# Kernel optimization log

Hardware: AMD Instinct MI355X
Metric: run time of the kernel (lower is better)

The kernel has to match this reference:

```python
import jax, jax.numpy as jnp
import numpy as np

N = 50000          # nodes
E = 800000         # edges (avg in-degree 16)
NFEAT, F = 128, 64 # input feat, hidden width (outfeat = outd_1 = outd_2 = 64)
ALPHA = 0.2        # leaky relu slope
AVG_LIN = 16.0             # sum(bin*hist)/N for deg histogram (all deg 16)
AVG_LOG = float(np.log(17.0))  # sum(log(bin+1)*hist)/N


def setup_inputs():
    key = jax.random.key(0)
    ks = jax.random.split(key, 16)
    g = lambda i, shp, s: (jax.random.normal(ks[i], shp, jnp.float32) * s)
    return {
        "x": g(0, (N, NFEAT), 1.0),
        "adj": jnp.zeros((1,), jnp.float32),
        "edge_index": jax.random.randint(ks[1], (2, E), 0, N, dtype=jnp.int32),
        "W0": g(2, (NFEAT, F), NFEAT ** -0.5), "b0": jnp.zeros((F,), jnp.float32),
        "c1_pre_W": g(3, (2 * F, F), (2 * F) ** -0.5), "c1_pre_b": jnp.zeros((F,), jnp.float32),
        "c1_post_W": g(4, (5 * F, F), (5 * F) ** -0.5), "c1_post_b": jnp.zeros((F,), jnp.float32),
        "c1_lin_W": g(5, (F, F), F ** -0.5), "c1_lin_b": jnp.zeros((F,), jnp.float32),
        "c2_pre_W": g(6, (2 * F, F), (2 * F) ** -0.5), "c2_pre_b": jnp.zeros((F,), jnp.float32),
        "c2_post_W": g(7, (5 * F, F), (5 * F) ** -0.5), "c2_post_b": jnp.zeros((F,), jnp.float32),
        "c2_lin_W": g(8, (F, F), F ** -0.5), "c2_lin_b": jnp.zeros((F,), jnp.float32),
        "W2": g(9, (F, 1), F ** -0.5), "b2": jnp.zeros((1,), jnp.float32),
    }


def pna_conv(x, src, dst, pre_W, pre_b, post_W, post_b, lin_W, lin_b):
    # message: pre_nn(cat[x_i, x_j]) per edge  (x_i = target, x_j = source)
    h = jnp.concatenate([x[dst], x[src]], axis=-1) @ pre_W + pre_b  # [E, F]
    cnt = jax.ops.segment_sum(jnp.ones((h.shape[0],), h.dtype), dst, num_segments=N)
    deg = jnp.clip(cnt, 1.0)                                        # [N]
    mean = jax.ops.segment_sum(h, dst, num_segments=N) / deg[:, None]
    mx = jax.ops.segment_max(h, dst, num_segments=N)
    mx = jnp.where(cnt[:, None] > 0, mx, 0.0)                       # empty segs -> 0
    agg = jnp.concatenate([mean, mx], axis=-1)                      # [N, 2F]
    att = agg * (AVG_LOG / jnp.log(deg + 1.0))[:, None]             # attenuation scaler
    lin = agg * (deg / AVG_LIN)[:, None]                            # linear scaler
    out = jnp.concatenate([x, att, lin], axis=-1)                   # [N, 5F]
    out = out @ post_W + post_b
    return out @ lin_W + lin_b


def reference(x, adj, edge_index, W0, b0,
              c1_pre_W, c1_pre_b, c1_post_W, c1_post_b, c1_lin_W, c1_lin_b,
              c2_pre_W, c2_pre_b, c2_post_W, c2_post_b, c2_lin_W, c2_lin_b,
              W2, b2):
    src, dst = edge_index[0], edge_index[1]
    h = jax.nn.leaky_relu(x @ W0 + b0, negative_slope=ALPHA)  # dropout = id (eval)
    h = jax.nn.relu(pna_conv(h, src, dst, c1_pre_W, c1_pre_b, c1_post_W, c1_post_b, c1_lin_W, c1_lin_b))
    h = jax.nn.relu(pna_conv(h, src, dst, c2_pre_W, c2_pre_b, c2_post_W, c2_post_b, c2_lin_W, c2_lin_b))
    return h @ W2 + b2  # [N, 1]
```

## Files before the change

kernel.cpp:

```cpp
#include <hip/hip_runtime.h>
#include <hip/hip_bf16.h>

typedef __hip_bfloat16 bf16;
typedef unsigned short u16;
typedef unsigned int u32;
typedef __attribute__((ext_vector_type(8))) short short8;
typedef __attribute__((ext_vector_type(4))) float f32x4;

static constexpr float AVG_LOG_C = 2.8332133440562162f;
#define BCAP 4096
#define CHUNK 8192

__device__ __forceinline__ u32 f2bf_bits(float f) {
    u32 u = __float_as_uint(f);
    return (u + 0x7fffu + ((u >> 16) & 1u)) >> 16;
}
__device__ __forceinline__ float bf2f(u16 b) {
    return __uint_as_float(((u32)b) << 16);
}

__global__ __launch_bounds__(1024) void detect_zero_kernel(
    const u32* __restrict__ xwords, int* __restrict__ flag,
    int* __restrict__ bcnt, int nb) {
    if (blockIdx.x == 0) {
        int tid = threadIdx.x;
        if (tid < 64) {
            int good = 0;
            for (int i = tid; i < 2048; i += 64) {
                u32 lo = xwords[i] & 0xffffu;
                float v = __uint_as_float(lo << 16);
                float a = fabsf(v);
                if (v == 0.0f || (a >= 1e-3f && a <= 100.0f)) good++;
            }
            for (int off = 32; off; off >>= 1) good += __shfl_xor(good, off, 64);
            if (tid == 0) *flag = (2 * good > 2048) ? 1 : 0;
        }
    } else {
        int i = (blockIdx.x - 1) * 1024 + threadIdx.x;
        if (i < nb) bcnt[i] = 0;
    }
}

__global__ void prep_kernel(
    const void* __restrict__ W0r,  const void* __restrict__ b0r,
    const void* __restrict__ pre1r, const void* __restrict__ preb1r,
    const void* __restrict__ post1r, const void* __restrict__ postb1r,
    const void* __restrict__ lin1r, const void* __restrict__ linb1r,
    const void* __restrict__ pre2r, const void* __restrict__ preb2r,
    const void* __restrict__ post2r, const void* __restrict__ postb2r,
    const void* __restrict__ lin2r, const void* __restrict__ linb2r,
    const void* __restrict__ W2r,  const void* __restrict__ b2r,
    u16* __restrict__ W0p, u16* __restrict__ pre1p, u16* __restrict__ pre2p,
    u16* __restrict__ wf1p, u16* __restrict__ wf2p,
    float* __restrict__ bfo1, float* __restrict__ bfo2,
    float* __restrict__ preb1f, float* __restrict__ preb2f,
    float* __restrict__ b0f, float* __restrict__ W2f, float* __restrict__ b2f,
    const int* __restrict__ flag) {
    int idx = blockIdx.x * 256 + threadIdx.x;
    bool isbf = (*flag) != 0;
    auto ld = [&](const void* p, int i) -> float {
        return isbf ? bf2f(((const u16*)p)[i]) : ((const float*)p)[i];
    };
    if (idx < 8192) {
        int j = idx & 7, l = (idx >> 3) & 63, tt = idx >> 9;
        int c = tt & 3, s = tt >> 2;
        int kk = s * 32 + (l >> 4) * 8 + j;
        int col = c * 16 + (l & 15);
        W0p[idx] = (u16)f2bf_bits(ld(W0r, kk * 64 + col));
        return;
    }
    idx -= 8192;
    for (int which = 0; which < 2; ++which) {
        if (idx < 8192) {
            const void* src = which ? pre2r : pre1r;
            u16* dst = which ? pre2p : pre1p;
            int j = idx & 7, l = (idx >> 3) & 63, tt = idx >> 9;
            int c = tt & 7, s = tt >> 3;
            int kk = s * 32 + (l >> 4) * 8 + j;
            int col = c * 16 + (l & 15);
            float v = (col < 64) ? ld(src, kk * 64 + col)
                                 : ld(src, (64 + kk) * 64 + (col - 64));
            dst[idx] = (u16)f2bf_bits(v);
            return;
        }
        idx -= 8192;
    }
    for (int which = 0; which < 2; ++which) {
        if (idx < 20480) {
            const void* postW = which ? post2r : post1r;
            const void* linW  = which ? lin2r  : lin1r;
            u16* dst = which ? wf2p : wf1p;
            int j = idx & 7, l = (idx >> 3) & 63, tt = idx >> 9;
            int c = tt & 3, s = tt >> 2;
            int kk = s * 32 + (l >> 4) * 8 + j;
            int col = c * 16 + (l & 15);
            float a = 0.f;
            for (int k = 0; k < 64; ++k)
                a = fmaf(ld(postW, kk * 64 + k), ld(linW, k * 64 + col), a);
            dst[idx] = (u16)f2bf_bits(a);
            return;
        }
        idx -= 20480;
    }
    for (int which = 0; which < 2; ++which) {
        if (idx < 64) {
            const void* postb = which ? postb2r : postb1r;
            const void* linW  = which ? lin2r : lin1r;
            const void* linb  = which ? linb2r : linb1r;
            float* dst = which ? bfo2 : bfo1;
            float a = ld(linb, idx);
            for (int k = 0; k < 64; ++k)
                a = fmaf(ld(postb, k), ld(linW, k * 64 + idx), a);
            dst[idx] = a;
            return;
        }
        idx -= 64;
    }
    if (idx < 64) { preb1f[idx] = ld(preb1r, idx); return; }
    idx -= 64;
    if (idx < 64) { preb2f[idx] = ld(preb2r, idx); return; }
    idx -= 64;
    if (idx < 64) { b0f[idx] = ld(b0r, idx); return; }
    idx -= 64;
    if (idx < 64) { W2f[idx] = ld(W2r, idx); return; }
    idx -= 64;
    if (idx < 1) { b2f[0] = ld(b2r, 0); }
}
#define PREP_TOTAL (8192 * 3 + 20480 * 2 + 64 * 6 + 1)

__global__ __launch_bounds__(1024) void bucket_scatter_kernel(
    const int* __restrict__ srcs, const int* __restrict__ dsts,
    int* __restrict__ bcnt, u32* __restrict__ bstage, int e, int nb) {
    __shared__ int lhist[1024];
    __shared__ int lbase[1024];
    int tid = threadIdx.x;
    int cbase = blockIdx.x * CHUNK;
    for (int b = tid; b < nb; b += 1024) lhist[b] = 0;
    __syncthreads();
#pragma unroll
    for (int i = 0; i < CHUNK; i += 1024) {
        int e0 = cbase + i + tid;
        if (e0 < e) atomicAdd(&lhist[dsts[e0] >> 7], 1);
    }
    __syncthreads();
    for (int b = tid; b < nb; b += 1024) {
        int c = lhist[b];
        lbase[b] = c ? atomicAdd(&bcnt[b], c) : 0;
        lhist[b] = 0;
    }
    __syncthreads();
#pragma unroll
    for (int i = 0; i < CHUNK; i += 1024) {
        int e0 = cbase + i + tid;
        if (e0 < e) {
            int d = dsts[e0];
            int b = d >> 7;
            int pos = lbase[b] + atomicAdd(&lhist[b], 1);
            if (pos < BCAP)
                bstage[(size_t)b * BCAP + pos] = (u32)srcs[e0] | ((u32)(d & 127) << 17);
        }
    }
}

__global__ __launch_bounds__(256) void bucket_build_kernel(
    const u32* __restrict__ bstage, const int* __restrict__ bcnt,
    int* __restrict__ rowptr, int* __restrict__ elist, int nb, int n) {
    __shared__ int hist[128];
    __shared__ int hoff[128];
    __shared__ int sbase;
    int b = blockIdx.x, tid = threadIdx.x;
    int lane = tid & 63;
    if (tid == 0) sbase = 0;
    if (tid < 128) hist[tid] = 0;
    __syncthreads();
    int part = 0;
    for (int k = tid; k < b; k += 256) part += min(bcnt[k], BCAP);
    for (int off = 32; off; off >>= 1) part += __shfl_xor(part, off, 64);
    if (lane == 0 && part) atomicAdd(&sbase, part);
    int cb = min(bcnt[b], BCAP);
    const u32* st = bstage + (size_t)b * BCAP;
    for (int i = tid; i < cb; i += 256) atomicAdd(&hist[st[i] >> 17], 1);
    __syncthreads();
    int base = sbase;
    if (tid == 0) {
        int run = 0;
        for (int j = 0; j < 128; ++j) { hoff[j] = run; run += hist[j]; }
    }
    __syncthreads();
    if (tid < 128) {
        int node = b * 128 + tid;
        if (node < n) rowptr[node] = base + hoff[tid];
        hist[tid] = hoff[tid];
    }
    if (b == nb - 1 && tid == 255) rowptr[n] = base + cb;
    __syncthreads();
    for (int i = tid; i < cb; i += 256) {
        u32 e = st[i];
        int pos = atomicAdd(&hist[e >> 17], 1);
        elist[base + pos] = (int)(e & 0x1ffffu);
    }
}

__global__ __launch_bounds__(1024) void gemm_x_pq_kernel(
    const void* __restrict__ xraw, const u16* __restrict__ W0p,
    const float* __restrict__ b0f, const u16* __restrict__ pre1p,
    u16* __restrict__ hA, u16* __restrict__ PQ,
    const int* __restrict__ flag, int n) {
    __shared__ __align__(16) u16 xsh[64 * 136];
    __shared__ __align__(16) u16 hsh[64 * 72];
    int tid = threadIdx.x;
    int wave = __builtin_amdgcn_readfirstlane(tid >> 6);
    int lane = tid & 63;
    int blockbase = blockIdx.x * 64;
    bool isbf = (*flag) != 0;
    {
        int row = tid >> 4;
        int cg = (tid & 15) * 8;
        int grow = blockbase + row;
        short8 v = short8{0, 0, 0, 0, 0, 0, 0, 0};
        if (grow < n) {
            if (isbf) {
                v = *(const short8*)((const u16*)xraw + (size_t)grow * 128 + cg);
            } else {
                const float* xf = (const float*)xraw + (size_t)grow * 128 + cg;
                f32x4 a0 = *(const f32x4*)xf;
                f32x4 a1 = *(const f32x4*)(xf + 4);
#pragma unroll
                for (int j = 0; j < 4; ++j) {
                    v[j]     = (short)f2bf_bits(a0[j]);
                    v[4 + j] = (short)f2bf_bits(a1[j]);
                }
            }
        }
        *(short8*)&xsh[row * 136 + cg] = v;
    }
    __syncthreads();
    int rt = wave & 3, ct = wave >> 2;
    int arl = rt * 16 + (lane & 15);
    int koff = (lane >> 4) * 8;
    f32x4 acc = f32x4{0.f, 0.f, 0.f, 0.f};
#pragma unroll
    for (int s = 0; s < 4; ++s) {
        short8 a = *(const short8*)&xsh[arl * 136 + s * 32 + koff];
        short8 b = *(const short8*)(W0p + ((size_t)(s * 4 + ct) * 64 + lane) * 8);
        acc = __builtin_amdgcn_mfma_f32_16x16x32_bf16(a, b, acc, 0, 0, 0);
    }
    {
        int col = ct * 16 + (lane & 15);
        float bv = b0f[col];
        int r0l = rt * 16 + (lane >> 4) * 4;
#pragma unroll
        for (int r = 0; r < 4; ++r) {
            float v = acc[r] + bv;
            v = v > 0.f ? v : 0.2f * v;
            u16 bits = (u16)f2bf_bits(v);
            hsh[(r0l + r) * 72 + col] = bits;
            int grow = blockbase + r0l + r;
            if (grow < n) hA[(size_t)grow * 64 + col] = bits;
        }
    }
    __syncthreads();
#pragma unroll
    for (int half = 0; half < 2; ++half) {
        int tile = wave * 2 + half;
        int rt2 = tile & 3, ct2 = tile >> 2;
        int ar2 = rt2 * 16 + (lane & 15);
        f32x4 acc2 = f32x4{0.f, 0.f, 0.f, 0.f};
#pragma unroll
        for (int s = 0; s < 2; ++s) {
            short8 a = *(const short8*)&hsh[ar2 * 72 + s * 32 + koff];
            short8 b = *(const short8*)(pre1p + ((size_t)(s * 8 + ct2) * 64 + lane) * 8);
            acc2 = __builtin_amdgcn_mfma_f32_16x16x32_bf16(a, b, acc2, 0, 0, 0);
        }
        int col2 = ct2 * 16 + (lane & 15);
        int r02 = rt2 * 16 + (lane >> 4) * 4;
#pragma unroll
        for (int r = 0; r < 4; ++r) {
            int grow = blockbase + r02 + r;
            if (grow < n) PQ[(size_t)grow * 128 + col2] = (u16)f2bf_bits(acc2[r]);
        }
    }
}

template<int FINAL>
__global__ __launch_bounds__(1024) void agg_gemm_kernel(
    const u16* __restrict__ PQ, const u16* __restrict__ h,
    const int* __restrict__ rowptr, const int* __restrict__ elist,
    const float* __restrict__ prebf, const u16* __restrict__ Wfp,
    const float* __restrict__ bfo, const u16* __restrict__ prenextp,
    u16* __restrict__ hout, u16* __restrict__ PQout,
    const float* __restrict__ W2f, const float* __restrict__ b2f,
    void* __restrict__ out, const int* __restrict__ flag, int n) {
    constexpr int PAD = 328;
    __shared__ __align__(16) u16 vsh[64 * PAD];
    __shared__ __align__(16) u16 hsh[64 * 72];
    __shared__ float fsum[64];
    int tid = threadIdx.x;
    int wave = __builtin_amdgcn_readfirstlane(tid >> 6);
    int lane = tid & 63;
    int blockbase = blockIdx.x * 64;
    float pbl = prebf[lane];
    if (FINAL && tid < 64) fsum[tid] = 0.f;
#pragma unroll
    for (int t = 0; t < 4; ++t) {
        int nl = wave * 4 + t;
        int node = blockbase + nl;
        u16* vrow = &vsh[nl * PAD];
        if (node < n) {
            int beg = rowptr[node], end = rowptr[node + 1];
            int cnt = end - beg;
            float s = 0.f, m = -3.4e38f;
            int e = beg;
            for (; e + 4 <= end; e += 4) {
                int s0 = elist[e], s1 = elist[e + 1], s2 = elist[e + 2], s3 = elist[e + 3];
                float q0 = bf2f(PQ[(size_t)s0 * 128 + 64 + lane]);
                float q1 = bf2f(PQ[(size_t)s1 * 128 + 64 + lane]);
                float q2 = bf2f(PQ[(size_t)s2 * 128 + 64 + lane]);
                float q3 = bf2f(PQ[(size_t)s3 * 128 + 64 + lane]);
                s += (q0 + q1) + (q2 + q3);
                m = fmaxf(fmaxf(m, fmaxf(q0, q1)), fmaxf(q2, q3));
            }
            for (; e < end; ++e) {
                float q = bf2f(PQ[(size_t)elist[e] * 128 + 64 + lane]);
                s += q;
                m = fmaxf(m, q);
            }
            float mean, mx, deg;
            if (cnt > 0) {
                deg = (float)cnt;
                float p = bf2f(PQ[(size_t)node * 128 + lane]) + pbl;
                mean = p + s / deg;
                mx = p + m;
            } else {
                deg = 1.f; mean = 0.f; mx = 0.f;
            }
            float att = AVG_LOG_C / logf(deg + 1.f);
            float lin = deg * (1.f / 16.f);
            vrow[lane]       = h[(size_t)node * 64 + lane];
            vrow[64 + lane]  = (u16)f2bf_bits(att * mean);
            vrow[128 + lane] = (u16)f2bf_bits(att * mx);
            vrow[192 + lane] = (u16)f2bf_bits(lin * mean);
            vrow[256 + lane] = (u16)f2bf_bits(lin * mx);
        } else {
            vrow[lane] = 0; vrow[64 + lane] = 0; vrow[128 + lane] = 0;
            vrow[192 + lane] = 0; vrow[256 + lane] = 0;
        }
    }
    __syncthreads();
    int rt = wave & 3, ct = wave >> 2;
    int arl = rt * 16 + (lane & 15);
    int koff = (lane >> 4) * 8;
    f32x4 acc = f32x4{0.f, 0.f, 0.f, 0.f};
#pragma unroll
    for (int s = 0; s < 10; ++s) {
        short8 a = *(const short8*)&vsh[arl * PAD + s * 32 + koff];
        short8 b = *(const short8*)(Wfp + ((size_t)(s * 4 + ct) * 64 + lane) * 8);
        acc = __builtin_amdgcn_mfma_f32_16x16x32_bf16(a, b, acc, 0, 0, 0);
    }
    int col = ct * 16 + (lane & 15);
    float bv = bfo[col];
    int r0l = rt * 16 + (lane >> 4) * 4;
    if constexpr (!FINAL) {
#pragma unroll
        for (int r = 0; r < 4; ++r) {
            float v = fmaxf(acc[r] + bv, 0.f);
            u16 bits = (u16)f2bf_bits(v);
            hsh[(r0l + r) * 72 + col] = bits;
            int grow = blockbase + r0l + r;
            if (grow < n) hout[(size_t)grow * 64 + col] = bits;
        }
        __syncthreads();
#pragma unroll
        for (int half = 0; half < 2; ++half) {
            int tile = wave * 2 + half;
            int rt2 = tile & 3, ct2 = tile >> 2;
            int ar2 = rt2 * 16 + (lane & 15);
            f32x4 acc2 = f32x4{0.f, 0.f, 0.f, 0.f};
#pragma unroll
            for (int s = 0; s < 2; ++s) {
                short8 a = *(const short8*)&hsh[ar2 * 72 + s * 32 + koff];
                short8 b = *(const short8*)(prenextp + ((size_t)(s * 8 + ct2) * 64 + lane) * 8);
                acc2 = __builtin_amdgcn_mfma_f32_16x16x32_bf16(a, b, acc2, 0, 0, 0);
            }
            int col2 = ct2 * 16 + (lane & 15);
            int r02 = rt2 * 16 + (lane >> 4) * 4;
#pragma unroll
            for (int r = 0; r < 4; ++r) {
                int grow = blockbase + r02 + r;
                if (grow < n) PQout[(size_t)grow * 128 + col2] = (u16)f2bf_bits(acc2[r]);
            }
        }
    } else {
        float w2 = W2f[col];
        float part[4];
#pragma unroll
        for (int r = 0; r < 4; ++r)
            part[r] = fmaxf(acc[r] + bv, 0.f) * w2;
#pragma unroll
        for (int r = 0; r < 4; ++r) {
            float v = part[r];
            v += __shfl_xor(v, 1, 64);
            v += __shfl_xor(v, 2, 64);
            v += __shfl_xor(v, 4, 64);
            v += __shfl_xor(v, 8, 64);
            if ((lane & 15) == 0) atomicAdd(&fsum[r0l + r], v);
        }
        __syncthreads();
        if (tid < 64) {
            int grow = blockbase + tid;
            if (grow < n) {
                float res = fsum[tid] + b2f[0];
                if (*flag) ((u16*)out)[grow] = (u16)f2bf_bits(res);
                else       ((float*)out)[grow] = res;
            }
        }
    }
}

extern "C" void kernel_launch(void* const* d_in, const int* in_sizes, int n_in,
                              void* d_out, int out_size, void* d_ws, size_t ws_size,
                              hipStream_t stream) {
    const int N = in_sizes[0] / 128;
    const int E = in_sizes[2] / 2;
    const int nb = (N + 127) >> 7;
    const int* ei = (const int*)d_in[2];
    const int* esrc = ei;
    const int* edst = ei + E;

    char* w = (char*)d_ws;
    auto alloc = [&](size_t bytes) -> void* {
        void* p = (void*)w;
        w += (bytes + 255) & ~(size_t)255;
        return p;
    };
    int* flag    = (int*)alloc(4);
    int* bcnt    = (int*)alloc((size_t)nb * 4);
    u32* bstage  = (u32*)alloc((size_t)nb * BCAP * 4);
    int* rowptr  = (int*)alloc((size_t)(N + 1) * 4);
    int* elist   = (int*)alloc((size_t)E * 4);
    u16* W0p     = (u16*)alloc(128 * 64 * 2);
    u16* pre1p   = (u16*)alloc(64 * 128 * 2);
    u16* pre2p   = (u16*)alloc(64 * 128 * 2);
    u16* wf1p    = (u16*)alloc(320 * 64 * 2);
    u16* wf2p    = (u16*)alloc(320 * 64 * 2);
    float* bfo1  = (float*)alloc(64 * 4);
    float* bfo2  = (float*)alloc(64 * 4);
    float* preb1f= (float*)alloc(64 * 4);
    float* preb2f= (float*)alloc(64 * 4);
    float* b0f   = (float*)alloc(64 * 4);
    float* W2f   = (float*)alloc(64 * 4);
    float* b2f_  = (float*)alloc(4);
    u16* hA      = (u16*)alloc((size_t)N * 64 * 2);
    u16* hB      = (u16*)alloc((size_t)N * 64 * 2);
    u16* PQA     = (u16*)alloc((size_t)N * 128 * 2);
    u16* PQB     = (u16*)alloc((size_t)N * 128 * 2);

    detect_zero_kernel<<<1 + (nb + 1023) / 1024, 1024, 0, stream>>>(
        (const u32*)d_in[0], flag, bcnt, nb);

    prep_kernel<<<(PREP_TOTAL + 255) / 256, 256, 0, stream>>>(
        d_in[3], d_in[4], d_in[5], d_in[6], d_in[7], d_in[8], d_in[9], d_in[10],
        d_in[11], d_in[12], d_in[13], d_in[14], d_in[15], d_in[16], d_in[17], d_in[18],
        W0p, pre1p, pre2p, wf1p, wf2p,
        bfo1, bfo2, preb1f, preb2f, b0f, W2f, b2f_, flag);

    bucket_scatter_kernel<<<(E + CHUNK - 1) / CHUNK, 1024, 0, stream>>>(
        esrc, edst, bcnt, bstage, E, nb);
    bucket_build_kernel<<<nb, 256, 0, stream>>>(bstage, bcnt, rowptr, elist, nb, N);

    int gblocks = (N + 63) / 64;
    gemm_x_pq_kernel<<<gblocks, 1024, 0, stream>>>(
        d_in[0], W0p, b0f, pre1p, hA, PQA, flag, N);

    agg_gemm_kernel<0><<<gblocks, 1024, 0, stream>>>(
        PQA, hA, rowptr, elist, preb1f, wf1p, bfo1, pre2p, hB, PQB,
        nullptr, nullptr, nullptr, flag, N);

    agg_gemm_kernel<1><<<gblocks, 1024, 0, stream>>>(
        PQB, hB, rowptr, elist, preb2f, wf2p, bfo2, nullptr, nullptr, nullptr,
        W2f, b2f_, d_out, flag, N);
}
```

Baseline: 224.2 us.

## Drop CSR build; sort edge buckets in shared memory inside aggregation kernels

Removes the separate bucket_build kernel and global rowptr/elist arrays. Each aggregation block now reads its own 64-node bucket from the staging buffer and does a local histogram, prefix scan and shared-memory counting sort. The edge scatter is merged into the weight-prep kernel, and the gather loop is unrolled by 8. Two launches go away, but the per-block sort runs twice (once per layer), and BCAP drops to 2048, which could truncate edges in dense buckets.

```diff
diff --git a/kernel.cpp b/kernel.cpp
--- a/kernel.cpp
+++ b/kernel.cpp
@@ -8,8 +8,9 @@
 typedef __attribute__((ext_vector_type(4))) float f32x4;
 
 static constexpr float AVG_LOG_C = 2.8332133440562162f;
-#define BCAP 4096
+#define BCAP 2048
 #define CHUNK 8192
+#define PREP_TOTAL (8192 * 3 + 20480 * 2 + 64 * 6 + 1)
 
 __device__ __forceinline__ u32 f2bf_bits(float f) {
     u32 u = __float_as_uint(f);
@@ -41,7 +42,9 @@
     }
 }
 
-__global__ void prep_kernel(
+__global__ __launch_bounds__(1024) void prep_scatter_kernel(
+    const int* __restrict__ srcs, const int* __restrict__ dsts,
+    int* __restrict__ bcnt, u32* __restrict__ bstage, int e, int nb,
     const void* __restrict__ W0r,  const void* __restrict__ b0r,
     const void* __restrict__ pre1r, const void* __restrict__ preb1r,
     const void* __restrict__ post1r, const void* __restrict__ postb1r,
@@ -56,7 +59,40 @@
     float* __restrict__ preb1f, float* __restrict__ preb2f,
     float* __restrict__ b0f, float* __restrict__ W2f, float* __restrict__ b2f,
     const int* __restrict__ flag) {
-    int idx = blockIdx.x * 256 + threadIdx.x;
+    __shared__ int lhist[1024];
+    __shared__ int lbase[1024];
+    int tid = threadIdx.x;
+    int scatB = (e + CHUNK - 1) / CHUNK;
+    if ((int)blockIdx.x < scatB) {
+        int cbase = blockIdx.x * CHUNK;
+        for (int b = tid; b < nb; b += 1024) lhist[b] = 0;
+        __syncthreads();
+#pragma unroll
+        for (int i = 0; i < CHUNK; i += 1024) {
+            int e0 = cbase + i + tid;
+            if (e0 < e) atomicAdd(&lhist[dsts[e0] >> 6], 1);
+        }
+        __syncthreads();
+        for (int b = tid; b < nb; b += 1024) {
+            int c = lhist[b];
+            lbase[b] = c ? atomicAdd(&bcnt[b], c) : 0;
+            lhist[b] = 0;
+        }
+        __syncthreads();
+#pragma unroll
+        for (int i = 0; i < CHUNK; i += 1024) {
+            int e0 = cbase + i + tid;
+            if (e0 < e) {
+                int d = dsts[e0];
+                int b = d >> 6;
+                int pos = lbase[b] + atomicAdd(&lhist[b], 1);
+                if (pos < BCAP)
+                    bstage[(size_t)b * BCAP + pos] = (u32)srcs[e0] | ((u32)(d & 63) << 17);
+            }
+        }
+        return;
+    }
+    int idx = ((int)blockIdx.x - scatB) * 1024 + tid;
     bool isbf = (*flag) != 0;
     auto ld = [&](const void* p, int i) -> float {
         return isbf ? bf2f(((const u16*)p)[i]) : ((const float*)p)[i];
@@ -125,80 +161,6 @@
     if (idx < 64) { W2f[idx] = ld(W2r, idx); return; }
     idx -= 64;
     if (idx < 1) { b2f[0] = ld(b2r, 0); }
-}
-#define PREP_TOTAL (8192 * 3 + 20480 * 2 + 64 * 6 + 1)
-
-__global__ __launch_bounds__(1024) void bucket_scatter_kernel(
-    const int* __restrict__ srcs, const int* __restrict__ dsts,
-    int* __restrict__ bcnt, u32* __restrict__ bstage, int e, int nb) {
-    __shared__ int lhist[1024];
-    __shared__ int lbase[1024];
-    int tid = threadIdx.x;
-    int cbase = blockIdx.x * CHUNK;
-    for (int b = tid; b < nb; b += 1024) lhist[b] = 0;
-    __syncthreads();
-#pragma unroll
-    for (int i = 0; i < CHUNK; i += 1024) {
-        int e0 = cbase + i + tid;
-        if (e0 < e) atomicAdd(&lhist[dsts[e0] >> 7], 1);
-    }
-    __syncthreads();
-    for (int b = tid; b < nb; b += 1024) {
-        int c = lhist[b];
-        lbase[b] = c ? atomicAdd(&bcnt[b], c) : 0;
-        lhist[b] = 0;
-    }
-    __syncthreads();
-#pragma unroll
-    for (int i = 0; i < CHUNK; i += 1024) {
-        int e0 = cbase + i + tid;
-        if (e0 < e) {
-            int d = dsts[e0];
-            int b = d >> 7;
-            int pos = lbase[b] + atomicAdd(&lhist[b], 1);
-            if (pos < BCAP)
-                bstage[(size_t)b * BCAP + pos] = (u32)srcs[e0] | ((u32)(d & 127) << 17);
-        }
-    }
-}
-
-__global__ __launch_bounds__(256) void bucket_build_kernel(
-    const u32* __restrict__ bstage, const int* __restrict__ bcnt,
-    int* __restrict__ rowptr, int* __restrict__ elist, int nb, int n) {
-    __shared__ int hist[128];
-    __shared__ int hoff[128];
-    __shared__ int sbase;
-    int b = blockIdx.x, tid = threadIdx.x;
-    int lane = tid & 63;
-    if (tid == 0) sbase = 0;
-    if (tid < 128) hist[tid] = 0;
-    __syncthreads();
-    int part = 0;
-    for (int k = tid; k < b; k += 256) part += min(bcnt[k], BCAP);
-    for (int off = 32; off; off >>= 1) part += __shfl_xor(part, off, 64);
-    if (lane == 0 && part) atomicAdd(&sbase, part);
-    int cb = min(bcnt[b], BCAP);
-    const u32* st = bstage + (size_t)b * BCAP;
-    for (int i = tid; i < cb; i += 256) atomicAdd(&hist[st[i] >> 17], 1);
-    __syncthreads();
-    int base = sbase;
-    if (tid == 0) {
-        int run = 0;
-        for (int j = 0; j < 128; ++j) { hoff[j] = run; run += hist[j]; }
-    }
-    __syncthreads();
-    if (tid < 128) {
-        int node = b * 128 + tid;
-        if (node < n) rowptr[node] = base + hoff[tid];
-        hist[tid] = hoff[tid];
-    }
-    if (b == nb - 1 && tid == 255) rowptr[n] = base + cb;
-    __syncthreads();
-    for (int i = tid; i < cb; i += 256) {
-        u32 e = st[i];
-        int pos = atomicAdd(&hist[e >> 17], 1);
-        elist[base + pos] = (int)(e & 0x1ffffu);
-    }
 }
 
 __global__ __launch_bounds__(1024) void gemm_x_pq_kernel(
@@ -285,7 +247,7 @@
 template<int FINAL>
 __global__ __launch_bounds__(1024) void agg_gemm_kernel(
     const u16* __restrict__ PQ, const u16* __restrict__ h,
-    const int* __restrict__ rowptr, const int* __restrict__ elist,
+    const u32* __restrict__ bstage, const int* __restrict__ bcnt,
     const float* __restrict__ prebf, const u16* __restrict__ Wfp,
     const float* __restrict__ bfo, const u16* __restrict__ prenextp,
     u16* __restrict__ hout, u16* __restrict__ PQout,
@@ -294,34 +256,72 @@
     constexpr int PAD = 328;
     __shared__ __align__(16) u16 vsh[64 * PAD];
     __shared__ __align__(16) u16 hsh[64 * 72];
+    __shared__ u32 lel[BCAP];
+    __shared__ int loff[64], lcnt[64], lcur[64];
     __shared__ float fsum[64];
     int tid = threadIdx.x;
     int wave = __builtin_amdgcn_readfirstlane(tid >> 6);
     int lane = tid & 63;
-    int blockbase = blockIdx.x * 64;
+    int b = blockIdx.x;
+    int blockbase = b * 64;
     float pbl = prebf[lane];
-    if (FINAL && tid < 64) fsum[tid] = 0.f;
+    if (tid < 64) { lcnt[tid] = 0; if (FINAL) fsum[tid] = 0.f; }
+    __syncthreads();
+    int cb = min(bcnt[b], BCAP);
+    const u32* st = bstage + (size_t)b * BCAP;
+    for (int i = tid; i < cb; i += 1024) atomicAdd(&lcnt[st[i] >> 17], 1);
+    __syncthreads();
+    if (wave == 0) {
+        int c = lcnt[lane];
+        int s = c;
+        for (int off = 1; off < 64; off <<= 1) {
+            int t = __shfl_up(s, (unsigned)off, 64);
+            if (lane >= off) s += t;
+        }
+        loff[lane] = s - c;
+        lcur[lane] = s - c;
+    }
+    __syncthreads();
+    for (int i = tid; i < cb; i += 1024) {
+        u32 e = st[i];
+        int pos = atomicAdd(&lcur[e >> 17], 1);
+        lel[pos] = e & 0x1ffffu;
+    }
+    __syncthreads();
+    const u16* Qb = PQ + 64 + lane;
 #pragma unroll
     for (int t = 0; t < 4; ++t) {
         int nl = wave * 4 + t;
         int node = blockbase + nl;
         u16* vrow = &vsh[nl * PAD];
         if (node < n) {
-            int beg = rowptr[node], end = rowptr[node + 1];
+            int beg = loff[nl], end = beg + lcnt[nl];
             int cnt = end - beg;
             float s = 0.f, m = -3.4e38f;
             int e = beg;
+            for (; e + 8 <= end; e += 8) {
+                float q0 = bf2f(Qb[(size_t)lel[e] * 128]);
+                float q1 = bf2f(Qb[(size_t)lel[e + 1] * 128]);
+                float q2 = bf2f(Qb[(size_t)lel[e + 2] * 128]);
+                float q3 = bf2f(Qb[(size_t)lel[e + 3] * 128]);
+                float q4 = bf2f(Qb[(size_t)lel[e + 4] * 128]);
+                float q5 = bf2f(Qb[(size_t)lel[e + 5] * 128]);
+                float q6 = bf2f(Qb[(size_t)lel[e + 6] * 128]);
+                float q7 = bf2f(Qb[(size_t)lel[e + 7] * 128]);
+                s += ((q0 + q1) + (q2 + q3)) + ((q4 + q5) + (q6 + q7));
+                m = fmaxf(m, fmaxf(fmaxf(fmaxf(q0, q1), fmaxf(q2, q3)),
+                                   fmaxf(fmaxf(q4, q5), fmaxf(q6, q7))));
+            }
             for (; e + 4 <= end; e += 4) {
-                int s0 = elist[e], s1 = elist[e + 1], s2 = elist[e + 2], s3 = elist[e + 3];
-                float q0 = bf2f(PQ[(size_t)s0 * 128 + 64 + lane]);
-                float q1 = bf2f(PQ[(size_t)s1 * 128 + 64 + lane]);
-                float q2 = bf2f(PQ[(size_t)s2 * 128 + 64 + lane]);
-                float q3 = bf2f(PQ[(size_t)s3 * 128 + 64 + lane]);
+                float q0 = bf2f(Qb[(size_t)lel[e] * 128]);
+                float q1 = bf2f(Qb[(size_t)lel[e + 1] * 128]);
+                float q2 = bf2f(Qb[(size_t)lel[e + 2] * 128]);
+                float q3 = bf2f(Qb[(size_t)lel[e + 3] * 128]);
                 s += (q0 + q1) + (q2 + q3);
                 m = fmaxf(fmaxf(m, fmaxf(q0, q1)), fmaxf(q2, q3));
             }
             for (; e < end; ++e) {
-                float q = bf2f(PQ[(size_t)elist[e] * 128 + 64 + lane]);
+                float q = bf2f(Qb[(size_t)lel[e] * 128]);
                 s += q;
                 m = fmaxf(m, q);
             }
@@ -354,8 +354,8 @@
 #pragma unroll
     for (int s = 0; s < 10; ++s) {
         short8 a = *(const short8*)&vsh[arl * PAD + s * 32 + koff];
-        short8 b = *(const short8*)(Wfp + ((size_t)(s * 4 + ct) * 64 + lane) * 8);
-        acc = __builtin_amdgcn_mfma_f32_16x16x32_bf16(a, b, acc, 0, 0, 0);
+        short8 b2 = *(const short8*)(Wfp + ((size_t)(s * 4 + ct) * 64 + lane) * 8);
+        acc = __builtin_amdgcn_mfma_f32_16x16x32_bf16(a, b2, acc, 0, 0, 0);
     }
     int col = ct * 16 + (lane & 15);
     float bv = bfo[col];
@@ -379,8 +379,8 @@
 #pragma unroll
             for (int s = 0; s < 2; ++s) {
                 short8 a = *(const short8*)&hsh[ar2 * 72 + s * 32 + koff];
-                short8 b = *(const short8*)(prenextp + ((size_t)(s * 8 + ct2) * 64 + lane) * 8);
-                acc2 = __builtin_amdgcn_mfma_f32_16x16x32_bf16(a, b, acc2, 0, 0, 0);
+                short8 b2 = *(const short8*)(prenextp + ((size_t)(s * 8 + ct2) * 64 + lane) * 8);
+                acc2 = __builtin_amdgcn_mfma_f32_16x16x32_bf16(a, b2, acc2, 0, 0, 0);
             }
             int col2 = ct2 * 16 + (lane & 15);
             int r02 = rt2 * 16 + (lane >> 4) * 4;
@@ -422,7 +422,7 @@
                               hipStream_t stream) {
     const int N = in_sizes[0] / 128;
     const int E = in_sizes[2] / 2;
-    const int nb = (N + 127) >> 7;
+    const int nb = (N + 63) >> 6;
     const int* ei = (const int*)d_in[2];
     const int* esrc = ei;
     const int* edst = ei + E;
@@ -436,8 +436,6 @@
     int* flag    = (int*)alloc(4);
     int* bcnt    = (int*)alloc((size_t)nb * 4);
     u32* bstage  = (u32*)alloc((size_t)nb * BCAP * 4);
-    int* rowptr  = (int*)alloc((size_t)(N + 1) * 4);
-    int* elist   = (int*)alloc((size_t)E * 4);
     u16* W0p     = (u16*)alloc(128 * 64 * 2);
     u16* pre1p   = (u16*)alloc(64 * 128 * 2);
     u16* pre2p   = (u16*)alloc(64 * 128 * 2);
@@ -458,25 +456,24 @@
     detect_zero_kernel<<<1 + (nb + 1023) / 1024, 1024, 0, stream>>>(
         (const u32*)d_in[0], flag, bcnt, nb);
 
-    prep_kernel<<<(PREP_TOTAL + 255) / 256, 256, 0, stream>>>(
+    int scatB = (E + CHUNK - 1) / CHUNK;
+    int prepB = (PREP_TOTAL + 1023) / 1024;
+    prep_scatter_kernel<<<scatB + prepB, 1024, 0, stream>>>(
+        esrc, edst, bcnt, bstage, E, nb,
         d_in[3], d_in[4], d_in[5], d_in[6], d_in[7], d_in[8], d_in[9], d_in[10],
         d_in[11], d_in[12], d_in[13], d_in[14], d_in[15], d_in[16], d_in[17], d_in[18],
         W0p, pre1p, pre2p, wf1p, wf2p,
         bfo1, bfo2, preb1f, preb2f, b0f, W2f, b2f_, flag);
 
-    bucket_scatter_kernel<<<(E + CHUNK - 1) / CHUNK, 1024, 0, stream>>>(
-        esrc, edst, bcnt, bstage, E, nb);
-    bucket_build_kernel<<<nb, 256, 0, stream>>>(bstage, bcnt, rowptr, elist, nb, N);
-
     int gblocks = (N + 63) / 64;
     gemm_x_pq_kernel<<<gblocks, 1024, 0, stream>>>(
         d_in[0], W0p, b0f, pre1p, hA, PQA, flag, N);
 
     agg_gemm_kernel<0><<<gblocks, 1024, 0, stream>>>(
-        PQA, hA, rowptr, elist, preb1f, wf1p, bfo1, pre2p, hB, PQB,
+        PQA, hA, bstage, bcnt, preb1f, wf1p, bfo1, pre2p, hB, PQB,
         nullptr, nullptr, nullptr, flag, N);
 
     agg_gemm_kernel<1><<<gblocks, 1024, 0, stream>>>(
-        PQB, hB, rowptr, elist, preb2f, wf2p, bfo2, nullptr, nullptr, nullptr,
+        PQB, hB, bstage, bcnt, preb2f, wf2p, bfo2, nullptr, nullptr, nullptr,
         W2f, b2f_, d_out, flag, N);
 }
```

Result: faster. 205.9 us (-8.2%).
